# Kernel tuning notes

Measured on AMD Instinct MI355X. Metric: run time of the kernel, lower is better.

Reference implementation:

```python
import jax, jax.numpy as jnp
import numpy as np

SIGMA = 1.0

def setup_inputs() -> dict:
    key = jax.random.key(0)
    kx, ky = jax.random.split(key)
    x = jax.random.normal(kx, (8192, 256), dtype=jnp.float32)
    y = jax.random.normal(ky, (8192, 256), dtype=jnp.float32)
    return {"x": x, "y": y}

def reference(x, y):
    x2 = jnp.sum(x * x, axis=-1)            # [N]
    y2 = jnp.sum(y * y, axis=-1)            # [M]
    d2 = x2[:, None] + y2[None, :] - 2.0 * (x @ y.T)  # [N, M]
    d2 = jnp.maximum(d2, 0.0)
    k = jnp.exp(-d2 / (2.0 * SIGMA ** 2))
    # original: exp(...)[None].sum(dim=0).mean() == mean over all N*M entries
    return jnp.mean(k)
```

## Files before the change

kernel.cpp:

```cpp
#include <hip/hip_runtime.h>
#include <hip/hip_fp8.h>

#define NROWS 8192
#define DIM   256

typedef float f32x4 __attribute__((ext_vector_type(4)));
typedef long  i64x2 __attribute__((ext_vector_type(2)));

typedef __attribute__((address_space(3))) char lds_char;
typedef __attribute__((address_space(1))) const char glob_char;

#define LOG2E  1.4426950408889634f
#define NEG_HALF_LOG2E (-0.7213475204444817f)

__device__ __forceinline__ int pack4_fp8(float a, float b, float c, float d) {
#if __has_builtin(__builtin_amdgcn_cvt_pk_fp8_f32)
    int pk = __builtin_amdgcn_cvt_pk_fp8_f32(a, b, 0, false);
    pk     = __builtin_amdgcn_cvt_pk_fp8_f32(c, d, pk, true);
    return pk;
#else
    union { unsigned char by[4]; int i; } u;
    u.by[0] = __hip_fp8_e4m3(a).__x;
    u.by[1] = __hip_fp8_e4m3(b).__x;
    u.by[2] = __hip_fp8_e4m3(c).__x;
    u.by[3] = __hip_fp8_e4m3(d).__x;
    return u.i;
#endif
}

__global__ __launch_bounds__(256) void prep_kernel(
    const float* __restrict__ x, const float* __restrict__ y,
    unsigned char* __restrict__ xb, unsigned char* __restrict__ yb,
    float* __restrict__ px, float* __restrict__ py,
    float* __restrict__ out)
{
    int tid  = threadIdx.x;
    int lane = tid & 63;
    int w    = tid >> 6;
    int row  = blockIdx.x * 4 + w;
    bool isx = row < NROWS;
    int r    = isx ? row : row - NROWS;
    const float* src = (isx ? x : y) + (size_t)r * DIM;
    float4 v = reinterpret_cast<const float4*>(src)[lane];
    float sq = v.x*v.x + v.y*v.y + v.z*v.z + v.w*v.w;
    #pragma unroll
    for (int off = 32; off; off >>= 1) sq += __shfl_xor(sq, off);

    int pk = pack4_fp8(v.x, v.y, v.z, v.w);
    int k0 = lane * 4;
    int kt = k0 >> 6, q = k0 & 63;
    int s  = q >> 5, hh = (q >> 3) & 3, j0 = q & 7;
    int p0 = (kt << 6) + (hh << 4) + (s << 3) + j0;
    unsigned char* dst = (isx ? xb : yb) + (size_t)r * DIM + p0;
    *reinterpret_cast<int*>(dst) = pk;

    if (lane == 0) (isx ? px : py)[r] = NEG_HALF_LOG2E * sq;
    if (blockIdx.x == 0 && tid == 0) out[0] = 0.0f;
}

__global__ __launch_bounds__(512, 4) void rbf_gemm_kernel(
    const unsigned char* __restrict__ xb, const unsigned char* __restrict__ yb,
    const float* __restrict__ px, const float* __restrict__ py,
    float* __restrict__ out)
{
    __shared__ __align__(16) char smem[49152];
    __shared__ float red[8];

    int tid  = threadIdx.x;
    int lane = tid & 63;
    int wv   = tid >> 6;
    int wm   = wv >> 1;
    int wn   = wv & 1;
    int b    = blockIdx.x;
    int bm   = (b & 7) * 4 + (b >> 9);
    int bn   = (b >> 3) & 63;
    int h    = lane >> 4;
    int l15  = lane & 15;

    f32x4 acc[4][4];
    #pragma unroll
    for (int m = 0; m < 4; ++m)
        #pragma unroll
        for (int n = 0; n < 4; ++n)
            acc[m][n] = (f32x4){0.f, 0.f, 0.f, 0.f};

    auto stage = [&](int buf, int kt) {
        char* base = smem + buf * 24576;
        #pragma unroll
        for (int j = 0; j < 2; ++j) {
            int e = j * 512 + tid;
            int hh = e >> 8, row = e & 255;
            __builtin_amdgcn_global_load_lds(
                (glob_char*)((const char*)xb + (size_t)(bm * 256 + row) * 256 + kt * 64 + hh * 16),
                (lds_char*)(base + e * 16), 16, 0, 0);
        }
        {
            int e = tid;
            int hh = e >> 7, row = e & 127;
            __builtin_amdgcn_global_load_lds(
                (glob_char*)((const char*)yb + (size_t)(bn * 128 + row) * 256 + kt * 64 + hh * 16),
                (lds_char*)(base + 16384 + e * 16), 16, 0, 0);
        }
    };

    auto compute = [&](int buf) {
        const char* Ab = smem + buf * 24576;
        const char* Bb = Ab + 16384;
        i64x2 aF[4], bF[4];
        #pragma unroll
        for (int mf = 0; mf < 4; ++mf)
            aF[mf] = *reinterpret_cast<const i64x2*>(
                Ab + h * 4096 + (wm * 64 + mf * 16 + l15) * 16);
        #pragma unroll
        for (int nf = 0; nf < 4; ++nf)
            bF[nf] = *reinterpret_cast<const i64x2*>(
                Bb + h * 2048 + (wn * 64 + nf * 16 + l15) * 16);
        __builtin_amdgcn_s_setprio(1);
        #pragma unroll
        for (int mf = 0; mf < 4; ++mf)
            #pragma unroll
            for (int nf = 0; nf < 4; ++nf) {
                acc[mf][nf] = __builtin_amdgcn_mfma_f32_16x16x32_fp8_fp8(
                    aF[mf][0], bF[nf][0], acc[mf][nf], 0, 0, 0);
                acc[mf][nf] = __builtin_amdgcn_mfma_f32_16x16x32_fp8_fp8(
                    aF[mf][1], bF[nf][1], acc[mf][nf], 0, 0, 0);
            }
        __builtin_amdgcn_s_setprio(0);
    };

    stage(0, 0);
    __syncthreads();
    #pragma unroll
    for (int kt = 0; kt < 4; ++kt) {
        int buf = kt & 1;
        if (kt < 3) stage(buf ^ 1, kt + 1);
        compute(buf);
        __syncthreads();
    }

    float lsum = 0.f;
    int colbase = bn * 128 + wn * 64 + l15;
    int rowbase = bm * 256 + wm * 64 + h * 4;
    float py4[4];
    #pragma unroll
    for (int nf = 0; nf < 4; ++nf) py4[nf] = py[colbase + nf * 16];
    #pragma unroll
    for (int mf = 0; mf < 4; ++mf) {
        #pragma unroll
        for (int r = 0; r < 4; ++r) {
            float pv = px[rowbase + mf * 16 + r];
            #pragma unroll
            for (int nf = 0; nf < 4; ++nf)
                lsum += exp2f(fmaf(acc[mf][nf][r], LOG2E, pv + py4[nf]));
        }
    }
    #pragma unroll
    for (int off = 32; off; off >>= 1) lsum += __shfl_xor(lsum, off);
    if (lane == 0) red[wv] = lsum;
    __syncthreads();
    if (tid == 0) {
        float s = (red[0] + red[1] + red[2] + red[3] +
                   red[4] + red[5] + red[6] + red[7]) * 1.4901161193847656e-08f;
        atomicAdd(out, s);
    }
}

extern "C" void kernel_launch(void* const* d_in, const int* in_sizes, int n_in,
                              void* d_out, int out_size, void* d_ws, size_t ws_size,
                              hipStream_t stream) {
    const float* x = (const float*)d_in[0];
    const float* y = (const float*)d_in[1];
    float* out = (float*)d_out;
    char* ws = (char*)d_ws;
    unsigned char* xb = (unsigned char*)ws;
    unsigned char* yb = (unsigned char*)(ws + (size_t)2 * 1024 * 1024);
    float* px = (float*)(ws + (size_t)4 * 1024 * 1024);
    float* py = (float*)(ws + (size_t)4 * 1024 * 1024 + 32 * 1024);

    hipLaunchKernelGGL(prep_kernel, dim3(4096), dim3(256), 0, stream,
                       x, y, xb, yb, px, py, out);
    hipLaunchKernelGGL(rbf_gemm_kernel, dim3(2048), dim3(512), 0, stream,
                       xb, yb, px, py, out);
}
```

Before: 116.1 us.

## Shrink GEMM block tile to 128x128 and stage row norms in LDS

Result: slower. 130.2 us (+12.1%).

```diff
diff --git a/kernel.cpp b/kernel.cpp
--- a/kernel.cpp
+++ b/kernel.cpp
@@ -58,100 +58,99 @@
     if (blockIdx.x == 0 && tid == 0) out[0] = 0.0f;
 }
 
-__global__ __launch_bounds__(512, 4) void rbf_gemm_kernel(
+__global__ __launch_bounds__(512, 6) void rbf_gemm_kernel(
     const unsigned char* __restrict__ xb, const unsigned char* __restrict__ yb,
     const float* __restrict__ px, const float* __restrict__ py,
     float* __restrict__ out)
 {
-    __shared__ __align__(16) char smem[49152];
-    __shared__ float red[8];
+    __shared__ __align__(16) char smem[33824];
+    float* pxl = (float*)(smem + 32768);
+    float* pyl = (float*)(smem + 33280);
+    float* red = (float*)(smem + 33792);
 
     int tid  = threadIdx.x;
     int lane = tid & 63;
     int wv   = tid >> 6;
-    int wm   = wv >> 1;
-    int wn   = wv & 1;
+    int wm   = wv >> 2;
+    int wn   = wv & 3;
     int b    = blockIdx.x;
-    int bm   = (b & 7) * 4 + (b >> 9);
-    int bn   = (b >> 3) & 63;
+    int c    = b & 7;
+    int s    = b >> 3;
+    int bm   = ((s >> 6) << 3) | c;
+    int bn   = s & 63;
     int h    = lane >> 4;
     int l15  = lane & 15;
 
-    f32x4 acc[4][4];
+    f32x4 acc[4][2];
     #pragma unroll
     for (int m = 0; m < 4; ++m)
         #pragma unroll
-        for (int n = 0; n < 4; ++n)
+        for (int n = 0; n < 2; ++n)
             acc[m][n] = (f32x4){0.f, 0.f, 0.f, 0.f};
 
     auto stage = [&](int buf, int kt) {
-        char* base = smem + buf * 24576;
-        #pragma unroll
-        for (int j = 0; j < 2; ++j) {
-            int e = j * 512 + tid;
-            int hh = e >> 8, row = e & 255;
-            __builtin_amdgcn_global_load_lds(
-                (glob_char*)((const char*)xb + (size_t)(bm * 256 + row) * 256 + kt * 64 + hh * 16),
-                (lds_char*)(base + e * 16), 16, 0, 0);
-        }
-        {
-            int e = tid;
-            int hh = e >> 7, row = e & 127;
-            __builtin_amdgcn_global_load_lds(
-                (glob_char*)((const char*)yb + (size_t)(bn * 128 + row) * 256 + kt * 64 + hh * 16),
-                (lds_char*)(base + 16384 + e * 16), 16, 0, 0);
-        }
+        char* base = smem + buf * 16384;
+        int hh = tid >> 7, row = tid & 127;
+        __builtin_amdgcn_global_load_lds(
+            (glob_char*)((const char*)xb + (size_t)(bm * 128 + row) * 256 + kt * 64 + hh * 16),
+            (lds_char*)(base + tid * 16), 16, 0, 0);
+        __builtin_amdgcn_global_load_lds(
+            (glob_char*)((const char*)yb + (size_t)(bn * 128 + row) * 256 + kt * 64 + hh * 16),
+            (lds_char*)(base + 8192 + tid * 16), 16, 0, 0);
     };
 
     auto compute = [&](int buf) {
-        const char* Ab = smem + buf * 24576;
-        const char* Bb = Ab + 16384;
-        i64x2 aF[4], bF[4];
+        const char* Ab = smem + buf * 16384;
+        const char* Bb = Ab + 8192;
+        i64x2 aF[4], bF[2];
         #pragma unroll
         for (int mf = 0; mf < 4; ++mf)
             aF[mf] = *reinterpret_cast<const i64x2*>(
-                Ab + h * 4096 + (wm * 64 + mf * 16 + l15) * 16);
+                Ab + h * 2048 + (wm * 64 + mf * 16 + l15) * 16);
         #pragma unroll
-        for (int nf = 0; nf < 4; ++nf)
+        for (int nf = 0; nf < 2; ++nf)
             bF[nf] = *reinterpret_cast<const i64x2*>(
-                Bb + h * 2048 + (wn * 64 + nf * 16 + l15) * 16);
-        __builtin_amdgcn_s_setprio(1);
+                Bb + h * 2048 + (wn * 32 + nf * 16 + l15) * 16);
         #pragma unroll
         for (int mf = 0; mf < 4; ++mf)
             #pragma unroll
-            for (int nf = 0; nf < 4; ++nf) {
+            for (int nf = 0; nf < 2; ++nf) {
                 acc[mf][nf] = __builtin_amdgcn_mfma_f32_16x16x32_fp8_fp8(
                     aF[mf][0], bF[nf][0], acc[mf][nf], 0, 0, 0);
                 acc[mf][nf] = __builtin_amdgcn_mfma_f32_16x16x32_fp8_fp8(
                     aF[mf][1], bF[nf][1], acc[mf][nf], 0, 0, 0);
             }
-        __builtin_amdgcn_s_setprio(0);
     };
 
+    if (tid < 128) {
+        __builtin_amdgcn_global_load_lds(
+            (glob_char*)((const char*)(px + bm * 128) + tid * 4),
+            (lds_char*)((char*)pxl + tid * 4), 4, 0, 0);
+        __builtin_amdgcn_global_load_lds(
+            (glob_char*)((const char*)(py + bn * 128) + tid * 4),
+            (lds_char*)((char*)pyl + tid * 4), 4, 0, 0);
+    }
     stage(0, 0);
     __syncthreads();
-    #pragma unroll
-    for (int kt = 0; kt < 4; ++kt) {
-        int buf = kt & 1;
-        if (kt < 3) stage(buf ^ 1, kt + 1);
-        compute(buf);
-        __syncthreads();
-    }
+
+    stage(1, 1); compute(0); __syncthreads();
+    stage(0, 2); compute(1); __syncthreads();
+    stage(1, 3); compute(0); __syncthreads();
+    compute(1);
 
     float lsum = 0.f;
-    int colbase = bn * 128 + wn * 64 + l15;
-    int rowbase = bm * 256 + wm * 64 + h * 4;
-    float py4[4];
+    float py2[2];
     #pragma unroll
-    for (int nf = 0; nf < 4; ++nf) py4[nf] = py[colbase + nf * 16];
+    for (int nf = 0; nf < 2; ++nf) py2[nf] = pyl[wn * 32 + nf * 16 + l15];
     #pragma unroll
     for (int mf = 0; mf < 4; ++mf) {
+        f32x4 pxv = *reinterpret_cast<const f32x4*>(pxl + wm * 64 + mf * 16 + h * 4);
         #pragma unroll
         for (int r = 0; r < 4; ++r) {
-            float pv = px[rowbase + mf * 16 + r];
+            float pv = pxv[r];
             #pragma unroll
-            for (int nf = 0; nf < 4; ++nf)
-                lsum += exp2f(fmaf(acc[mf][nf][r], LOG2E, pv + py4[nf]));
+            for (int nf = 0; nf < 2; ++nf)
+                lsum += exp2f(fmaf(acc[mf][nf][r], LOG2E, pv + py2[nf]));
         }
     }
     #pragma unroll
@@ -159,9 +158,9 @@
     if (lane == 0) red[wv] = lsum;
     __syncthreads();
     if (tid == 0) {
-        float s = (red[0] + red[1] + red[2] + red[3] +
-                   red[4] + red[5] + red[6] + red[7]) * 1.4901161193847656e-08f;
-        atomicAdd(out, s);
+        float ss = (red[0] + red[1] + red[2] + red[3] +
+                    red[4] + red[5] + red[6] + red[7]) * 1.4901161193847656e-08f;
+        atomicAdd(out, ss);
     }
 }
 
@@ -179,6 +178,6 @@
 
     hipLaunchKernelGGL(prep_kernel, dim3(4096), dim3(256), 0, stream,
                        x, y, xb, yb, px, py, out);
-    hipLaunchKernelGGL(rbf_gemm_kernel, dim3(2048), dim3(512), 0, stream,
+    hipLaunchKernelGGL(rbf_gemm_kernel, dim3(4096), dim3(512), 0, stream,
                        xb, yb, px, py, out);
 }
```
